# Kernel tuning notes

Measured on AMD Instinct MI355X. Metric: run time of the kernel, lower is better.

Reference implementation:

```python
import jax, jax.numpy as jnp
import numpy as np

B, T, HID = 2, 2048, 1024
H, DK, DV = 8, 128, 128      # num_heads, head_f_dim (key), head_i_dim (value)
LR = 128                     # gate low-rank dim
EPS = 1e-5


def setup_inputs() -> dict:
    key = jax.random.key(0)
    ks = jax.random.split(key, 8)
    def w(k, shape, fan_in):
        return jax.random.normal(k, shape, jnp.float32) / np.float32(np.sqrt(fan_in))
    return {
        "hidden_states": jax.random.normal(ks[0], (B, T, HID), jnp.float32),
        "Wq": w(ks[1], (HID, HID), HID),   # key_dim x hidden
        "Wk": w(ks[2], (HID, HID), HID),
        "Wv": w(ks[3], (HID, HID), HID),   # value_dim x hidden
        "Wg1": w(ks[4], (LR, HID), HID),   # low-rank gate down
        "Wg2": w(ks[5], (HID, LR), LR),    # low-rank gate up
        "g_norm_weight": jnp.ones((HID,), jnp.float32),
        "Wo": w(ks[6], (HID, HID), HID),
    }


def _lightnet_fwd(x, Wq, Wk, Wv, Wg1, Wg2, g_norm_weight, Wo):
    b, t, _ = x.shape
    q = jax.nn.silu(x @ Wq.T).reshape(b, t, H, DK)
    k = (x @ Wk.T).reshape(b, t, H, DK)
    v = (x @ Wv.T).reshape(b, t, H, DV)

    # LightNet gating: normalized keys via logcumsumexp over time
    z = jax.lax.cumlogsumexp(k, axis=1)                 # [b,t,h,dk]
    k = jnp.exp(k - z)                                  # exp-normalized keys
    g = jnp.concatenate([z[:, :1], z[:, :-1]], axis=1) - z  # <= 0; g[:,0]=0

    scale = DK ** -0.5

    # gated linear attention recurrence: S_t = exp(g_t) * S_{t-1} + k_t v_t^T
    def step(S, inp):
        qt, kt, vt, gt = inp                            # [b,h,dk],[b,h,dk],[b,h,dv],[b,h,dk]
        S = jnp.exp(gt)[..., None] * S + kt[..., None] * vt[..., None, :]
        o = jnp.einsum('bhk,bhkv->bhv', qt, S) * scale
        return S, o

    S0 = jnp.zeros((b, H, DK, DV), x.dtype)
    tfirst = lambda a: jnp.moveaxis(a, 1, 0)
    _, oT = jax.lax.scan(step, S0, (tfirst(q), tfirst(k), tfirst(v), tfirst(g)))
    o = jnp.moveaxis(oT, 0, 1).reshape(b, t, H * DV)    # [b,t,hidden]

    # RMSNorm(o) * swish(gate) then output projection
    gate = (x @ Wg1.T) @ Wg2.T
    o = o * jax.lax.rsqrt(jnp.mean(o * o, axis=-1, keepdims=True) + EPS) * g_norm_weight
    o = o * gate * jax.nn.sigmoid(gate)
    return o @ Wo.T


def reference(hidden_states, Wq, Wk, Wv, Wg1, Wg2, g_norm_weight, Wo):
    return _lightnet_fwd(hidden_states, Wq, Wk, Wv, Wg1, Wg2, g_norm_weight, Wo)
```

## Files before the change

### kernel.cpp

```cpp
#include <hip/hip_runtime.h>
#include <hip/hip_bf16.h>
#include <stdint.h>


typedef short short8 __attribute__((ext_vector_type(8)));
typedef float f32x4 __attribute__((ext_vector_type(4)));

#define T_SEQ 2048
#define HIDN  1024
#define SCALE 0.08838834764831845f
#define LDSP  136

__device__ __forceinline__ float blo(unsigned int u){
  union{unsigned int i; float f;} v; v.i = u << 16; return v.f;
}
__device__ __forceinline__ float bhi(unsigned int u){
  union{unsigned int i; float f;} v; v.i = u & 0xffff0000u; return v.f;
}
__device__ __forceinline__ float bu2f(unsigned short u){
  union{unsigned int i; float f;} v; v.i = ((unsigned int)u) << 16; return v.f;
}
__device__ __forceinline__ unsigned short f2bu(float f){
  union{float f; unsigned int i;} v; v.f = f;
  unsigned int x = v.i;
  x += 0x7fffu + ((x >> 16) & 1u);
  return (unsigned short)(x >> 16);
}
__device__ __forceinline__ void up8(const unsigned short* p, float* f){
  uint4 v = *(const uint4*)p;
  f[0]=blo(v.x); f[1]=bhi(v.x); f[2]=blo(v.y); f[3]=bhi(v.y);
  f[4]=blo(v.z); f[5]=bhi(v.z); f[6]=blo(v.w); f[7]=bhi(v.w);
}
__device__ __forceinline__ void async16(const void* g, void* l){
  __builtin_amdgcn_global_load_lds(
      (const __attribute__((address_space(1))) unsigned int*)g,
      (__attribute__((address_space(3))) unsigned int*)l, 16, 0, 0);
}

__global__ __launch_bounds__(256) void convert_all(
    const float* __restrict__ X,  const float* __restrict__ Wq,
    const float* __restrict__ Wk, const float* __restrict__ Wv,
    const float* __restrict__ Wg1,const float* __restrict__ Wg2,
    const float* __restrict__ gnw,const float* __restrict__ Wo,
    unsigned short* __restrict__ base)
{
  int q = blockIdx.x * 256 + threadIdx.x;
  const float* src; unsigned short* dst; int rel = q;
  if (rel < 1048576)            { src = X;   dst = base;            }
  else if ((rel -= 1048576) < 262144) { src = Wq;  dst = base + 4194304; }
  else if ((rel -=  262144) < 262144) { src = Wk;  dst = base + 5242880; }
  else if ((rel -=  262144) < 262144) { src = Wv;  dst = base + 6291456; }
  else if ((rel -=  262144) < 262144) { src = Wo;  dst = base + 7340032; }
  else if ((rel -=  262144) <  32768) { src = Wg1; dst = base + 8388608; }
  else if ((rel -=   32768) <  32768) { src = Wg2; dst = base + 8519680; }
  else   { rel -= 32768;                src = gnw; dst = base + 8650752; }
  float4 v = ((const float4*)src)[rel];
  ushort4 o; o.x=f2bu(v.x); o.y=f2bu(v.y); o.z=f2bu(v.z); o.w=f2bu(v.w);
  ((ushort4*)dst)[rel] = o;
}

__device__ __forceinline__ void gemm_core(
    const unsigned short* __restrict__ A, const unsigned short* __restrict__ B,
    int K, int row0, int col0,
    unsigned short* sA, unsigned short* sB, f32x4 acc[4][4], int tid)
{
  const int lane = tid & 63;
  const int wm = (tid >> 6) & 1, wn = tid >> 7;
  const int wb = tid & 192;
  for (int k0 = 0; k0 < K; k0 += 32){
    __syncthreads();
#pragma unroll
    for (int r = 0; r < 2; ++r){
      int idx  = r*256 + tid;
      int mrow = idx >> 2, kc = (idx & 3) * 8;
      async16(A + (size_t)(row0 + mrow)*K + k0 + kc, sA + (size_t)(r*256 + wb)*8);
      async16(B + (size_t)(col0 + mrow)*K + k0 + kc, sB + (size_t)(r*256 + wb)*8);
    }
    __syncthreads();
    short8 av[4], bv[4];
#pragma unroll
    for (int i=0;i<4;i++)
      av[i] = *(const short8*)(sA + (size_t)(wm*64 + i*16 + (lane&15))*32 + (lane>>4)*8);
#pragma unroll
    for (int j=0;j<4;j++)
      bv[j] = *(const short8*)(sB + (size_t)(wn*64 + j*16 + (lane&15))*32 + (lane>>4)*8);
#pragma unroll
    for (int i=0;i<4;i++)
#pragma unroll
      for (int j=0;j<4;j++)
        acc[i][j] = __builtin_amdgcn_mfma_f32_16x16x32_bf16(av[i], bv[j], acc[i][j], 0, 0, 0);
  }
}

__device__ __forceinline__ void epilogue_lds(
    f32x4 acc[4][4], int row0, int col0, int tid, int ldc, int act,
    unsigned short* __restrict__ Cb, unsigned short* sC)
{
  const int lane = tid & 63;
  const int wm = (tid >> 6) & 1, wn = tid >> 7;
#pragma unroll
  for (int p=0;p<4;p++){
    __syncthreads();
    if (wm == (p>>1)){
#pragma unroll
      for (int ii=0; ii<2; ii++){
        int i = (p&1)*2 + ii;
        int lr = i*16 + ((lane>>4)<<2) - (p&1)*32;
#pragma unroll
        for (int j=0;j<4;j++){
          int col = wn*64 + j*16 + (lane&15);
#pragma unroll
          for (int r=0;r<4;r++){
            float v = acc[i][j][r];
            if (act) v = v / (1.f + __expf(-v));
            sC[(lr+r)*128 + col] = f2bu(v);
          }
        }
      }
    }
    __syncthreads();
#pragma unroll
    for (int c = tid; c < 512; c += 256){
      int rr = c >> 4, off = (c & 15)*8;
      *(uint4*)&Cb[(size_t)(row0 + p*32 + rr)*ldc + col0 + off] =
          *(const uint4*)&sC[rr*128 + off];
    }
  }
}

__device__ __forceinline__ void epilogue_f32(
    f32x4 acc[4][4], int row0, int col0, int tid, int ldc,
    float* __restrict__ Cf)
{
  const int lane = tid & 63;
  const int wm = (tid >> 6) & 1, wn = tid >> 7;
#pragma unroll
  for (int i=0;i<4;i++){
    int rbase = row0 + wm*64 + i*16 + ((lane>>4)<<2);
#pragma unroll
    for (int j=0;j<4;j++){
      int col = col0 + wn*64 + j*16 + (lane&15);
#pragma unroll
      for (int r=0;r<4;r++)
        Cf[(size_t)(rbase + r)*ldc + col] = acc[i][j][r];
    }
  }
}

__global__ __launch_bounds__(256, 2) void proj_kernel(
    const unsigned short* __restrict__ X,
    const unsigned short* __restrict__ Wq, const unsigned short* __restrict__ Wk,
    const unsigned short* __restrict__ Wv, const unsigned short* __restrict__ Wg1,
    unsigned short* __restrict__ Qb, unsigned short* __restrict__ Kb,
    unsigned short* __restrict__ Vb, unsigned short* __restrict__ G1b)
{
  __shared__ unsigned short sA[128*32], sB[128*32];
  int tid = threadIdx.x;
  int which = blockIdx.y >> 3;
  const unsigned short* Bp = (which==0)?Wq:(which==1)?Wk:(which==2)?Wv:Wg1;
  int row0 = blockIdx.x * 128;
  int col0 = (which==3) ? 0 : (blockIdx.y & 7) * 128;
  f32x4 acc[4][4] = {};
  gemm_core(X, Bp, HIDN, row0, col0, sA, sB, acc, tid);
  if      (which==0) epilogue_lds(acc,row0,col0,tid,HIDN,1,Qb, sA);
  else if (which==1) epilogue_lds(acc,row0,col0,tid,HIDN,0,Kb, sA);
  else if (which==2) epilogue_lds(acc,row0,col0,tid,HIDN,0,Vb, sA);
  else               epilogue_lds(acc,row0,col0,tid,128 ,0,G1b,sA);
}

__global__ __launch_bounds__(256, 2) void gemm_bt(
    const unsigned short* __restrict__ A, const unsigned short* __restrict__ B,
    int K, int ldc, int act, float* __restrict__ Cf,
    unsigned short* __restrict__ Cb)
{
  __shared__ unsigned short sA[128*32], sB[128*32];
  int tid = threadIdx.x;
  int row0 = blockIdx.x * 128, col0 = blockIdx.y * 128;
  f32x4 acc[4][4] = {};
  gemm_core(A, B, K, row0, col0, sA, sB, acc, tid);
  if (Cb) epilogue_lds(acc, row0, col0, tid, ldc, act, Cb, sA);
  else    epilogue_f32(acc, row0, col0, tid, ldc, Cf);
}

__global__ __launch_bounds__(256) void attn_pass1(
    const unsigned short* __restrict__ Kb, const unsigned short* __restrict__ Vb,
    unsigned short* __restrict__ U, float* __restrict__ Esum)
{
  __shared__ unsigned short se[128*128];
  __shared__ unsigned short sv[128*128];
  int tid = threadIdx.x;
  int bh = blockIdx.x >> 4, ch = blockIdx.x & 15;
  int b = bh >> 3, h = bh & 7;
  size_t rowbase = (size_t)(b*T_SEQ + ch*128)*HIDN + h*128;

#pragma unroll
  for (int i=0;i<8;i++){
    int u = tid + i*256; int t = u >> 4, kc = (u & 15)*8;
    float kv[8]; up8(&Kb[rowbase + (size_t)t*HIDN + kc], kv);
    ushort4 a, c;
    a.x=f2bu(__expf(kv[0])); a.y=f2bu(__expf(kv[1]));
    a.z=f2bu(__expf(kv[2])); a.w=f2bu(__expf(kv[3]));
    c.x=f2bu(__expf(kv[4])); c.y=f2bu(__expf(kv[5]));
    c.z=f2bu(__expf(kv[6])); c.w=f2bu(__expf(kv[7]));
    *(ushort4*)&se[t*128 + kc    ] = a;
    *(ushort4*)&se[t*128 + kc + 4] = c;
  }
#pragma unroll
  for (int i=0;i<8;i++){
    int u = tid + i*256; int t = u >> 4, kc = (u & 15)*8;
    ((uint4*)sv)[u] = *(const uint4*)&Vb[rowbase + (size_t)t*HIDN + kc];
  }
  __syncthreads();

  if (tid < 128){
    float s = 0.f;
#pragma unroll 8
    for (int t=0;t<128;t++) s += bu2f(se[t*128 + tid]);
    Esum[(size_t)blockIdx.x*128 + tid] = s;
  }

  int kg = tid >> 4, vg = tid & 15;
  int k0 = kg*8, v0 = vg*8;
  float uacc[8][8] = {};
  for (int s=0;s<128;s++){
    float ev[8], vv[8];
    up8(&se[s*128 + k0], ev);
    up8(&sv[s*128 + v0], vv);
#pragma unroll
    for (int i=0;i<8;i++)
#pragma unroll
      for (int j=0;j<8;j++) uacc[i][j] += ev[i]*vv[j];
  }
  unsigned short* Ub = U + (size_t)blockIdx.x*16384;
#pragma unroll
  for (int j=0;j<8;j++){
    ushort4 w0, w1;
    w0.x=f2bu(uacc[0][j]); w0.y=f2bu(uacc[1][j]); w0.z=f2bu(uacc[2][j]); w0.w=f2bu(uacc[3][j]);
    w1.x=f2bu(uacc[4][j]); w1.y=f2bu(uacc[5][j]); w1.z=f2bu(uacc[6][j]); w1.w=f2bu(uacc[7][j]);
    *(ushort4*)&Ub[(v0+j)*128 + k0    ] = w0;
    *(ushort4*)&Ub[(v0+j)*128 + k0 + 4] = w1;
  }
}

__global__ __launch_bounds__(256) void attn_pass2(
    unsigned short* __restrict__ U, float* __restrict__ Esum)
{
  int bh = blockIdx.x >> 4, sl = blockIdx.x & 15;
  int p = sl*1024 + threadIdx.x*4;
  float r0=0.f, r1=0.f, r2=0.f, r3=0.f;
  for (int c=0;c<16;c++){
    ushort4* ptr = (ushort4*)&U[(size_t)(bh*16 + c)*16384 + p];
    ushort4 t = *ptr;
    ushort4 w;
    w.x=f2bu(r0); w.y=f2bu(r1); w.z=f2bu(r2); w.w=f2bu(r3);
    *ptr = w;
    r0 += bu2f(t.x); r1 += bu2f(t.y); r2 += bu2f(t.z); r3 += bu2f(t.w);
  }
  if (sl == 0 && threadIdx.x < 128){
    float r = 0.f;
    for (int c=0;c<16;c++){
      float* q = &Esum[(size_t)(bh*16 + c)*128 + threadIdx.x];
      float t = *q; *q = r; r += t;
    }
  }
}

__global__ __launch_bounds__(512, 2) void attn_pass3(
    const unsigned short* __restrict__ Kb, const unsigned short* __restrict__ Qb,
    const unsigned short* __restrict__ Vb, const unsigned short* __restrict__ U,
    const float* __restrict__ Esum, unsigned short* __restrict__ Oatt)
{
  __shared__ unsigned short smem[3*128*LDSP];
  __shared__ float seg_part[4*128];
  unsigned short* bufA = smem;
  unsigned short* bufB = smem + 128*LDSP;
  unsigned short* bufC = smem + 2*128*LDSP;

  int tid = threadIdx.x;
  const int lane = tid & 63, quad = lane >> 4;
  const int w = tid >> 6, wm = w & 3, wn = w >> 2;
  const int Rb = wm*32, Cb = wn*64;
  int bh = blockIdx.x >> 4, ch = blockIdx.x & 15;
  int b = bh >> 3, h = bh & 7;
  size_t rowbase = (size_t)(b*T_SEQ + ch*128)*HIDN + h*128;

#pragma unroll
  for (int i=0;i<4;i++){
    int u = tid + i*512; int t = u >> 4, kc = (u & 15)*8;
    *(uint4*)&bufA[t*LDSP + kc] = *(const uint4*)&Qb[rowbase + (size_t)t*HIDN + kc];
    float kv[8]; up8(&Kb[rowbase + (size_t)t*HIDN + kc], kv);
    ushort4 a, c;
    a.x=f2bu(__expf(kv[0])); a.y=f2bu(__expf(kv[1]));
    a.z=f2bu(__expf(kv[2])); a.w=f2bu(__expf(kv[3]));
    c.x=f2bu(__expf(kv[4])); c.y=f2bu(__expf(kv[5]));
    c.z=f2bu(__expf(kv[6])); c.w=f2bu(__expf(kv[7]));
    *(ushort4*)&bufB[t*LDSP + kc    ] = a;
    *(ushort4*)&bufB[t*LDSP + kc + 4] = c;
    *(uint4*)&bufC[t*LDSP + kc] =
        *(const uint4*)&U[(size_t)blockIdx.x*16384 + (size_t)t*128 + kc];
  }
  __syncthreads();

  {
    int col = tid & 127, seg = tid >> 7;
    float psum = 0.f;
    for (int s = seg*32; s < seg*32+32; ++s) psum += bu2f(bufB[s*LDSP + col]);
    seg_part[seg*128 + col] = psum;
    __syncthreads();
    float run = Esum[(size_t)blockIdx.x*128 + col];
    for (int ss=0; ss<4; ++ss) if (ss < seg) run += seg_part[ss*128 + col];
    for (int s = seg*32; s < seg*32+32; ++s){
      run += bu2f(bufB[s*LDSP + col]);
      float q = bu2f(bufA[s*LDSP + col]);
      bufA[s*LDSP + col] = f2bu(q * SCALE * __builtin_amdgcn_rcpf(run));
    }
  }
  __syncthreads();

  f32x4 accO[2][4] = {}, accP[2][4] = {};
  short8 av[2], bv[4];
#pragma unroll
  for (int k0=0; k0<128; k0+=32){
#pragma unroll
    for (int i=0;i<2;i++)
      av[i] = *(const short8*)(bufA + (Rb + i*16 + (lane&15))*LDSP + k0 + quad*8);
#pragma unroll
    for (int j=0;j<4;j++)
      bv[j] = *(const short8*)(bufC + (Cb + j*16 + (lane&15))*LDSP + k0 + quad*8);
#pragma unroll
    for (int i=0;i<2;i++)
#pragma unroll
      for (int j=0;j<4;j++)
        accO[i][j] = __builtin_amdgcn_mfma_f32_16x16x32_bf16(av[i], bv[j], accO[i][j], 0,0,0);
#pragma unroll
    for (int j=0;j<4;j++)
      bv[j] = *(const short8*)(bufB + (Cb + j*16 + (lane&15))*LDSP + k0 + quad*8);
#pragma unroll
    for (int i=0;i<2;i++)
#pragma unroll
      for (int j=0;j<4;j++)
        accP[i][j] = __builtin_amdgcn_mfma_f32_16x16x32_bf16(av[i], bv[j], accP[i][j], 0,0,0);
  }
  __syncthreads();

#pragma unroll
  for (int i=0;i<2;i++){
#pragma unroll
    for (int j=0;j<4;j++){
      int s = Cb + j*16 + (lane&15);
#pragma unroll
      for (int r=0;r<4;r++){
        int t = Rb + i*16 + quad*4 + r;
        bufA[t*LDSP + s] = f2bu(s <= t ? accP[i][j][r] : 0.f);
      }
    }
  }
#pragma unroll
  for (int i=0;i<4;i++){
    int u = tid + i*512; int t = u >> 4, kc = (u & 15)*8;
    unsigned short tmp[8];
    *(uint4*)tmp = *(const uint4*)&Vb[rowbase + (size_t)t*HIDN + kc];
#pragma unroll
    for (int j=0;j<8;j++) bufB[(kc+j)*LDSP + t] = tmp[j];
  }
  __syncthreads();

#pragma unroll
  for (int k0=0; k0<128; k0+=32){
#pragma unroll
    for (int i=0;i<2;i++)
      av[i] = *(const short8*)(bufA + (Rb + i*16 + (lane&15))*LDSP + k0 + quad*8);
#pragma unroll
    for (int j=0;j<4;j++)
      bv[j] = *(const short8*)(bufB + (Cb + j*16 + (lane&15))*LDSP + k0 + quad*8);
#pragma unroll
    for (int i=0;i<2;i++)
#pragma unroll
      for (int j=0;j<4;j++)
        accO[i][j] = __builtin_amdgcn_mfma_f32_16x16x32_bf16(av[i], bv[j], accO[i][j], 0,0,0);
  }
  __syncthreads();

#pragma unroll
  for (int i=0;i<2;i++){
#pragma unroll
    for (int j=0;j<4;j++){
      int v = Cb + j*16 + (lane&15);
#pragma unroll
      for (int r=0;r<4;r++){
        int t = Rb + i*16 + quad*4 + r;
        bufC[t*LDSP + v] = f2bu(accO[i][j][r]);
      }
    }
  }
  __syncthreads();
#pragma unroll
  for (int i=0;i<4;i++){
    int u = tid + i*512; int t = u >> 4, kc = (u & 15)*8;
    *(uint4*)&Oatt[rowbase + (size_t)t*HIDN + kc] = *(const uint4*)&bufC[t*LDSP + kc];
  }
}

__global__ __launch_bounds__(256) void norm_gate(
    const unsigned short* __restrict__ Oatt, const unsigned short* __restrict__ Gt,
    const unsigned short* __restrict__ gnw, unsigned short* __restrict__ Onorm)
{
  int row = blockIdx.x, tid = threadIdx.x;
  ushort4 o4 = *(const ushort4*)&Oatt[(size_t)row*HIDN + tid*4];
  float ox = bu2f(o4.x), oy = bu2f(o4.y), oz = bu2f(o4.z), ow = bu2f(o4.w);
  float ss = ox*ox + oy*oy + oz*oz + ow*ow;
#pragma unroll
  for (int off=32; off>0; off>>=1) ss += __shfl_down(ss, off, 64);
  __shared__ float red[4];
  if ((tid & 63) == 0) red[tid>>6] = ss;
  __syncthreads();
  float rstd = rsqrtf((red[0]+red[1]+red[2]+red[3]) * (1.f/1024.f) + 1e-5f);
  ushort4 g4 = *(const ushort4*)&Gt[(size_t)row*HIDN + tid*4];
  ushort4 w4 = *(const ushort4*)&gnw[tid*4];
  ushort4 r4;
  r4.x = f2bu(ox * rstd * bu2f(w4.x) * bu2f(g4.x));
  r4.y = f2bu(oy * rstd * bu2f(w4.y) * bu2f(g4.y));
  r4.z = f2bu(oz * rstd * bu2f(w4.z) * bu2f(g4.z));
  r4.w = f2bu(ow * rstd * bu2f(w4.w) * bu2f(g4.w));
  *(ushort4*)&Onorm[(size_t)row*HIDN + tid*4] = r4;
}

extern "C" void kernel_launch(void* const* d_in, const int* in_sizes, int n_in,
                              void* d_out, int out_size, void* d_ws, size_t ws_size,
                              hipStream_t stream) {
  unsigned short* wsS = (unsigned short*)d_ws;

  unsigned short* Xc   = wsS;
  unsigned short* Wqc  = wsS + 4194304;
  unsigned short* Wkc  = wsS + 5242880;
  unsigned short* Wvc  = wsS + 6291456;
  unsigned short* Woc  = wsS + 7340032;
  unsigned short* Wg1c = wsS + 8388608;
  unsigned short* Wg2c = wsS + 8519680;
  unsigned short* gnwc = wsS + 8650752;
  unsigned short* Qb   = wsS + 8651776;
  unsigned short* Kb   = wsS + 12846080;
  unsigned short* Vb   = wsS + 17040384;
  unsigned short* G1b  = wsS + 21234688;
  unsigned short* Gt   = wsS + 21758976;
  unsigned short* Ub   = wsS + 25953280;
  unsigned short* Oattb= wsS + 30147584;
  float*          Esum = (float*)(wsS + 34341888);
  unsigned short* Onorm = Qb;

  convert_all<<<8449, 256, 0, stream>>>(
      (const float*)d_in[0], (const float*)d_in[1], (const float*)d_in[2],
      (const float*)d_in[3], (const float*)d_in[4], (const float*)d_in[5],
      (const float*)d_in[6], (const float*)d_in[7], wsS);

  proj_kernel<<<dim3(32,25), 256, 0, stream>>>(Xc, Wqc, Wkc, Wvc, Wg1c, Qb, Kb, Vb, G1b);
  gemm_bt   <<<dim3(32,8),  256, 0, stream>>>(G1b, Wg2c, 128, HIDN, 1, nullptr, Gt);
  attn_pass1<<<256, 256, 0, stream>>>(Kb, Vb, Ub, Esum);
  attn_pass2<<<256, 256, 0, stream>>>(Ub, Esum);
  attn_pass3<<<256, 512, 0, stream>>>(Kb, Qb, Vb, Ub, Esum, Oattb);
  norm_gate <<<4096, 256, 0, stream>>>(Oattb, Gt, gnwc, Onorm);
  gemm_bt   <<<dim3(32,8),  256, 0, stream>>>(Onorm, Woc, HIDN, HIDN, 0,
                                              (float*)d_out, nullptr);
}
```

Baseline: 223.5 us.

## Fuse RMSNorm-gate into output GEMM, MFMA-ize chunk state pass, widen GEMM K-tile

The output GEMM now applies the RMSNorm, gnorm weight and gate while staging its A operand. The per-row sum of squares is accumulated with atomics in attn_pass3, and convert_all zeroes the buffer first, so the separate norm_gate kernel and its round trip through global memory go away. attn_pass1's chunk outer product is rewritten from scalar FMA loops over LDS into MFMA on transposed tiles with 512 threads. The shared GEMM core loads a 64-wide K tile per barrier pair instead of 32, halving the number of syncs. Costs: the A tile in out_gemm is loaded synchronously with elementwise math, LDS per block doubles in the GEMMs, and atomic accumulation makes the sum-of-squares order non-deterministic.

Result: no change. 223.6 us (+0.1%).

```diff
diff --git a/kernel.cpp b/kernel.cpp
--- a/kernel.cpp
+++ b/kernel.cpp
@@ -42,7 +42,7 @@
     const float* __restrict__ Wk, const float* __restrict__ Wv,
     const float* __restrict__ Wg1,const float* __restrict__ Wg2,
     const float* __restrict__ gnw,const float* __restrict__ Wo,
-    unsigned short* __restrict__ base)
+    unsigned short* __restrict__ base, float* __restrict__ SumSq)
 {
   int q = blockIdx.x * 256 + threadIdx.x;
   const float* src; unsigned short* dst; int rel = q;
@@ -53,7 +53,9 @@
   else if ((rel -=  262144) < 262144) { src = Wo;  dst = base + 7340032; }
   else if ((rel -=  262144) <  32768) { src = Wg1; dst = base + 8388608; }
   else if ((rel -=   32768) <  32768) { src = Wg2; dst = base + 8519680; }
-  else   { rel -= 32768;                src = gnw; dst = base + 8650752; }
+  else if ((rel -=   32768) <    256) { src = gnw; dst = base + 8650752; }
+  else { rel -= 256;
+    ((float4*)SumSq)[rel] = make_float4(0.f,0.f,0.f,0.f); return; }
   float4 v = ((const float4*)src)[rel];
   ushort4 o; o.x=f2bu(v.x); o.y=f2bu(v.y); o.z=f2bu(v.z); o.w=f2bu(v.w);
   ((ushort4*)dst)[rel] = o;
@@ -67,28 +69,36 @@
   const int lane = tid & 63;
   const int wm = (tid >> 6) & 1, wn = tid >> 7;
   const int wb = tid & 192;
-  for (int k0 = 0; k0 < K; k0 += 32){
-    __syncthreads();
-#pragma unroll
-    for (int r = 0; r < 2; ++r){
-      int idx  = r*256 + tid;
-      int mrow = idx >> 2, kc = (idx & 3) * 8;
-      async16(A + (size_t)(row0 + mrow)*K + k0 + kc, sA + (size_t)(r*256 + wb)*8);
-      async16(B + (size_t)(col0 + mrow)*K + k0 + kc, sB + (size_t)(r*256 + wb)*8);
-    }
-    __syncthreads();
-    short8 av[4], bv[4];
-#pragma unroll
-    for (int i=0;i<4;i++)
-      av[i] = *(const short8*)(sA + (size_t)(wm*64 + i*16 + (lane&15))*32 + (lane>>4)*8);
-#pragma unroll
-    for (int j=0;j<4;j++)
-      bv[j] = *(const short8*)(sB + (size_t)(wn*64 + j*16 + (lane&15))*32 + (lane>>4)*8);
-#pragma unroll
-    for (int i=0;i<4;i++)
+  for (int k0 = 0; k0 < K; k0 += 64){
+    __syncthreads();
+#pragma unroll
+    for (int h = 0; h < 2; ++h){
+#pragma unroll
+      for (int r = 0; r < 2; ++r){
+        int idx  = r*256 + tid;
+        int mrow = idx >> 2, kc = (idx & 3) * 8;
+        async16(A + (size_t)(row0 + mrow)*K + k0 + h*32 + kc,
+                sA + (size_t)(h*512 + r*256 + wb)*8);
+        async16(B + (size_t)(col0 + mrow)*K + k0 + h*32 + kc,
+                sB + (size_t)(h*512 + r*256 + wb)*8);
+      }
+    }
+    __syncthreads();
+#pragma unroll
+    for (int h = 0; h < 2; ++h){
+      short8 av[4], bv[4];
+#pragma unroll
+      for (int i=0;i<4;i++)
+        av[i] = *(const short8*)(sA + h*4096 + (size_t)(wm*64 + i*16 + (lane&15))*32 + (lane>>4)*8);
 #pragma unroll
       for (int j=0;j<4;j++)
-        acc[i][j] = __builtin_amdgcn_mfma_f32_16x16x32_bf16(av[i], bv[j], acc[i][j], 0, 0, 0);
+        bv[j] = *(const short8*)(sB + h*4096 + (size_t)(wn*64 + j*16 + (lane&15))*32 + (lane>>4)*8);
+#pragma unroll
+      for (int i=0;i<4;i++)
+#pragma unroll
+        for (int j=0;j<4;j++)
+          acc[i][j] = __builtin_amdgcn_mfma_f32_16x16x32_bf16(av[i], bv[j], acc[i][j], 0, 0, 0);
+    }
   }
 }
 
@@ -154,7 +164,7 @@
     unsigned short* __restrict__ Qb, unsigned short* __restrict__ Kb,
     unsigned short* __restrict__ Vb, unsigned short* __restrict__ G1b)
 {
-  __shared__ unsigned short sA[128*32], sB[128*32];
+  __shared__ unsigned short sA[128*64], sB[128*64];
   int tid = threadIdx.x;
   int which = blockIdx.y >> 3;
   const unsigned short* Bp = (which==0)?Wq:(which==1)?Wk:(which==2)?Wv:Wg1;
@@ -170,75 +180,143 @@
 
 __global__ __launch_bounds__(256, 2) void gemm_bt(
     const unsigned short* __restrict__ A, const unsigned short* __restrict__ B,
-    int K, int ldc, int act, float* __restrict__ Cf,
-    unsigned short* __restrict__ Cb)
-{
-  __shared__ unsigned short sA[128*32], sB[128*32];
+    int K, int ldc, int act, unsigned short* __restrict__ Cb)
+{
+  __shared__ unsigned short sA[128*64], sB[128*64];
   int tid = threadIdx.x;
   int row0 = blockIdx.x * 128, col0 = blockIdx.y * 128;
   f32x4 acc[4][4] = {};
   gemm_core(A, B, K, row0, col0, sA, sB, acc, tid);
-  if (Cb) epilogue_lds(acc, row0, col0, tid, ldc, act, Cb, sA);
-  else    epilogue_f32(acc, row0, col0, tid, ldc, Cf);
-}
-
-__global__ __launch_bounds__(256) void attn_pass1(
+  epilogue_lds(acc, row0, col0, tid, ldc, act, Cb, sA);
+}
+
+__global__ __launch_bounds__(256, 2) void out_gemm(
+    const unsigned short* __restrict__ Oatt, const unsigned short* __restrict__ Gt,
+    const unsigned short* __restrict__ gnw,  const float* __restrict__ SumSq,
+    const unsigned short* __restrict__ Wo,   float* __restrict__ Out)
+{
+  __shared__ unsigned short sA[128*64], sB[128*64];
+  int tid = threadIdx.x;
+  int row0 = blockIdx.x * 128, col0 = blockIdx.y * 128;
+  const int wb = tid & 192;
+  f32x4 acc[4][4] = {};
+  const int lane = tid & 63;
+  const int wm = (tid >> 6) & 1, wn = tid >> 7;
+  for (int k0 = 0; k0 < HIDN; k0 += 64){
+    __syncthreads();
+#pragma unroll
+    for (int h = 0; h < 2; ++h){
+#pragma unroll
+      for (int r = 0; r < 2; ++r){
+        int idx  = r*256 + tid;
+        int mrow = idx >> 2, kc = (idx & 3) * 8;
+        async16(Wo + (size_t)(col0 + mrow)*HIDN + k0 + h*32 + kc,
+                sB + (size_t)(h*512 + r*256 + wb)*8);
+        int grow = row0 + mrow, gcol = k0 + h*32 + kc;
+        float o[8], g[8], w[8];
+        up8(&Oatt[(size_t)grow*HIDN + gcol], o);
+        up8(&Gt  [(size_t)grow*HIDN + gcol], g);
+        up8(&gnw[gcol], w);
+        float rstd = rsqrtf(SumSq[grow]*(1.f/1024.f) + 1e-5f);
+        unsigned short a8[8];
+#pragma unroll
+        for (int j=0;j<8;j++) a8[j] = f2bu(o[j]*rstd*w[j]*g[j]);
+        *(uint4*)(sA + (size_t)(h*4096 + mrow*32 + kc)) = *(const uint4*)a8;
+      }
+    }
+    __syncthreads();
+#pragma unroll
+    for (int h = 0; h < 2; ++h){
+      short8 av[4], bv[4];
+#pragma unroll
+      for (int i=0;i<4;i++)
+        av[i] = *(const short8*)(sA + h*4096 + (size_t)(wm*64 + i*16 + (lane&15))*32 + (lane>>4)*8);
+#pragma unroll
+      for (int j=0;j<4;j++)
+        bv[j] = *(const short8*)(sB + h*4096 + (size_t)(wn*64 + j*16 + (lane&15))*32 + (lane>>4)*8);
+#pragma unroll
+      for (int i=0;i<4;i++)
+#pragma unroll
+        for (int j=0;j<4;j++)
+          acc[i][j] = __builtin_amdgcn_mfma_f32_16x16x32_bf16(av[i], bv[j], acc[i][j], 0, 0, 0);
+    }
+  }
+  epilogue_f32(acc, row0, col0, tid, HIDN, Out);
+}
+
+__global__ __launch_bounds__(512, 2) void attn_pass1(
     const unsigned short* __restrict__ Kb, const unsigned short* __restrict__ Vb,
     unsigned short* __restrict__ U, float* __restrict__ Esum)
 {
-  __shared__ unsigned short se[128*128];
-  __shared__ unsigned short sv[128*128];
+  __shared__ unsigned short Vt[128*LDSP], Et[128*LDSP];
+  __shared__ float seg_part[4*128];
   int tid = threadIdx.x;
+  const int lane = tid & 63, quad = lane >> 4;
+  const int w = tid >> 6, wm = w & 3, wn = w >> 2;
+  const int Rb = wm*32, Cb = wn*64;
   int bh = blockIdx.x >> 4, ch = blockIdx.x & 15;
   int b = bh >> 3, h = bh & 7;
   size_t rowbase = (size_t)(b*T_SEQ + ch*128)*HIDN + h*128;
 
 #pragma unroll
-  for (int i=0;i<8;i++){
-    int u = tid + i*256; int t = u >> 4, kc = (u & 15)*8;
+  for (int i=0;i<4;i++){
+    int u = tid + i*512; int t = u >> 4, kc = (u & 15)*8;
+    unsigned short tmp[8];
+    *(uint4*)tmp = *(const uint4*)&Vb[rowbase + (size_t)t*HIDN + kc];
+#pragma unroll
+    for (int j=0;j<8;j++) Vt[(kc+j)*LDSP + t] = tmp[j];
     float kv[8]; up8(&Kb[rowbase + (size_t)t*HIDN + kc], kv);
-    ushort4 a, c;
-    a.x=f2bu(__expf(kv[0])); a.y=f2bu(__expf(kv[1]));
-    a.z=f2bu(__expf(kv[2])); a.w=f2bu(__expf(kv[3]));
-    c.x=f2bu(__expf(kv[4])); c.y=f2bu(__expf(kv[5]));
-    c.z=f2bu(__expf(kv[6])); c.w=f2bu(__expf(kv[7]));
-    *(ushort4*)&se[t*128 + kc    ] = a;
-    *(ushort4*)&se[t*128 + kc + 4] = c;
-  }
-#pragma unroll
-  for (int i=0;i<8;i++){
-    int u = tid + i*256; int t = u >> 4, kc = (u & 15)*8;
-    ((uint4*)sv)[u] = *(const uint4*)&Vb[rowbase + (size_t)t*HIDN + kc];
-  }
-  __syncthreads();
-
-  if (tid < 128){
+#pragma unroll
+    for (int j=0;j<8;j++) Et[(kc+j)*LDSP + t] = f2bu(__expf(kv[j]));
+  }
+  __syncthreads();
+
+  {
+    int seg = tid >> 7, k = tid & 127;
     float s = 0.f;
-#pragma unroll 8
-    for (int t=0;t<128;t++) s += bu2f(se[t*128 + tid]);
-    Esum[(size_t)blockIdx.x*128 + tid] = s;
-  }
-
-  int kg = tid >> 4, vg = tid & 15;
-  int k0 = kg*8, v0 = vg*8;
-  float uacc[8][8] = {};
-  for (int s=0;s<128;s++){
-    float ev[8], vv[8];
-    up8(&se[s*128 + k0], ev);
-    up8(&sv[s*128 + v0], vv);
-#pragma unroll
-    for (int i=0;i<8;i++)
-#pragma unroll
-      for (int j=0;j<8;j++) uacc[i][j] += ev[i]*vv[j];
-  }
+    for (int c = seg*32; c < seg*32+32; ++c) s += bu2f(Et[k*LDSP + c]);
+    seg_part[seg*128 + k] = s;
+  }
+  __syncthreads();
+  if (tid < 128)
+    Esum[(size_t)blockIdx.x*128 + tid] =
+        seg_part[tid] + seg_part[128+tid] + seg_part[256+tid] + seg_part[384+tid];
+
+  f32x4 acc[2][4] = {};
+  short8 av[2], bv[4];
+#pragma unroll
+  for (int s0=0; s0<128; s0+=32){
+#pragma unroll
+    for (int i=0;i<2;i++)
+      av[i] = *(const short8*)(Vt + (Rb + i*16 + (lane&15))*LDSP + s0 + quad*8);
+#pragma unroll
+    for (int j=0;j<4;j++)
+      bv[j] = *(const short8*)(Et + (Cb + j*16 + (lane&15))*LDSP + s0 + quad*8);
+#pragma unroll
+    for (int i=0;i<2;i++)
+#pragma unroll
+      for (int j=0;j<4;j++)
+        acc[i][j] = __builtin_amdgcn_mfma_f32_16x16x32_bf16(av[i], bv[j], acc[i][j], 0,0,0);
+  }
+  __syncthreads();
+
+#pragma unroll
+  for (int i=0;i<2;i++)
+#pragma unroll
+    for (int j=0;j<4;j++){
+      int k = Cb + j*16 + (lane&15);
+#pragma unroll
+      for (int r=0;r<4;r++){
+        int v = Rb + i*16 + quad*4 + r;
+        Et[v*LDSP + k] = f2bu(acc[i][j][r]);
+      }
+    }
+  __syncthreads();
   unsigned short* Ub = U + (size_t)blockIdx.x*16384;
 #pragma unroll
-  for (int j=0;j<8;j++){
-    ushort4 w0, w1;
-    w0.x=f2bu(uacc[0][j]); w0.y=f2bu(uacc[1][j]); w0.z=f2bu(uacc[2][j]); w0.w=f2bu(uacc[3][j]);
-    w1.x=f2bu(uacc[4][j]); w1.y=f2bu(uacc[5][j]); w1.z=f2bu(uacc[6][j]); w1.w=f2bu(uacc[7][j]);
-    *(ushort4*)&Ub[(v0+j)*128 + k0    ] = w0;
-    *(ushort4*)&Ub[(v0+j)*128 + k0 + 4] = w1;
+  for (int i=0;i<4;i++){
+    int u = tid + i*512; int v = u >> 4, kc = (u & 15)*8;
+    *(uint4*)&Ub[v*128 + kc] = *(const uint4*)&Et[v*LDSP + kc];
   }
 }
 
@@ -268,7 +346,8 @@
 __global__ __launch_bounds__(512, 2) void attn_pass3(
     const unsigned short* __restrict__ Kb, const unsigned short* __restrict__ Qb,
     const unsigned short* __restrict__ Vb, const unsigned short* __restrict__ U,
-    const float* __restrict__ Esum, unsigned short* __restrict__ Oatt)
+    const float* __restrict__ Esum, unsigned short* __restrict__ Oatt,
+    float* __restrict__ SumSq)
 {
   __shared__ unsigned short smem[3*128*LDSP];
   __shared__ float seg_part[4*128];
@@ -394,35 +473,25 @@
     }
   }
   __syncthreads();
+
+  {
+    int seg = tid >> 7, row = tid & 127;
+    float s = 0.f;
+    for (int c = seg*32; c < seg*32+32; ++c){
+      float x = bu2f(bufC[row*LDSP + c]); s += x*x;
+    }
+    seg_part[seg*128 + row] = s;
+  }
 #pragma unroll
   for (int i=0;i<4;i++){
     int u = tid + i*512; int t = u >> 4, kc = (u & 15)*8;
     *(uint4*)&Oatt[rowbase + (size_t)t*HIDN + kc] = *(const uint4*)&bufC[t*LDSP + kc];
   }
-}
-
-__global__ __launch_bounds__(256) void norm_gate(
-    const unsigned short* __restrict__ Oatt, const unsigned short* __restrict__ Gt,
-    const unsigned short* __restrict__ gnw, unsigned short* __restrict__ Onorm)
-{
-  int row = blockIdx.x, tid = threadIdx.x;
-  ushort4 o4 = *(const ushort4*)&Oatt[(size_t)row*HIDN + tid*4];
-  float ox = bu2f(o4.x), oy = bu2f(o4.y), oz = bu2f(o4.z), ow = bu2f(o4.w);
-  float ss = ox*ox + oy*oy + oz*oz + ow*ow;
-#pragma unroll
-  for (int off=32; off>0; off>>=1) ss += __shfl_down(ss, off, 64);
-  __shared__ float red[4];
-  if ((tid & 63) == 0) red[tid>>6] = ss;
-  __syncthreads();
-  float rstd = rsqrtf((red[0]+red[1]+red[2]+red[3]) * (1.f/1024.f) + 1e-5f);
-  ushort4 g4 = *(const ushort4*)&Gt[(size_t)row*HIDN + tid*4];
-  ushort4 w4 = *(const ushort4*)&gnw[tid*4];
-  ushort4 r4;
-  r4.x = f2bu(ox * rstd * bu2f(w4.x) * bu2f(g4.x));
-  r4.y = f2bu(oy * rstd * bu2f(w4.y) * bu2f(g4.y));
-  r4.z = f2bu(oz * rstd * bu2f(w4.z) * bu2f(g4.z));
-  r4.w = f2bu(ow * rstd * bu2f(w4.w) * bu2f(g4.w));
-  *(ushort4*)&Onorm[(size_t)row*HIDN + tid*4] = r4;
+  __syncthreads();
+  if (tid < 128){
+    float s = seg_part[tid] + seg_part[128+tid] + seg_part[256+tid] + seg_part[384+tid];
+    atomicAdd(&SumSq[(size_t)b*T_SEQ + ch*128 + tid], s);
+  }
 }
 
 extern "C" void kernel_launch(void* const* d_in, const int* in_sizes, int n_in,
@@ -446,19 +515,18 @@
   unsigned short* Ub   = wsS + 25953280;
   unsigned short* Oattb= wsS + 30147584;
   float*          Esum = (float*)(wsS + 34341888);
-  unsigned short* Onorm = Qb;
-
-  convert_all<<<8449, 256, 0, stream>>>(
+  float*          SumSq= (float*)(wsS + 34407424);
+
+  convert_all<<<8453, 256, 0, stream>>>(
       (const float*)d_in[0], (const float*)d_in[1], (const float*)d_in[2],
       (const float*)d_in[3], (const float*)d_in[4], (const float*)d_in[5],
-      (const float*)d_in[6], (const float*)d_in[7], wsS);
+      (const float*)d_in[6], (const float*)d_in[7], wsS, SumSq);
 
   proj_kernel<<<dim3(32,25), 256, 0, stream>>>(Xc, Wqc, Wkc, Wvc, Wg1c, Qb, Kb, Vb, G1b);
-  gemm_bt   <<<dim3(32,8),  256, 0, stream>>>(G1b, Wg2c, 128, HIDN, 1, nullptr, Gt);
-  attn_pass1<<<256, 256, 0, stream>>>(Kb, Vb, Ub, Esum);
+  gemm_bt   <<<dim3(32,8),  256, 0, stream>>>(G1b, Wg2c, 128, HIDN, 1, Gt);
+  attn_pass1<<<256, 512, 0, stream>>>(Kb, Vb, Ub, Esum);
   attn_pass2<<<256, 256, 0, stream>>>(Ub, Esum);
-  attn_pass3<<<256, 512, 0, stream>>>(Kb, Qb, Vb, Ub, Esum, Oattb);
-  norm_gate <<<4096, 256, 0, stream>>>(Oattb, Gt, gnwc, Onorm);
-  gemm_bt   <<<dim3(32,8),  256, 0, stream>>>(Onorm, Woc, HIDN, HIDN, 0,
-                                              (float*)d_out, nullptr);
-}
+  attn_pass3<<<256, 512, 0, stream>>>(Kb, Qb, Vb, Ub, Esum, Oattb, SumSq);
+  out_gemm  <<<dim3(32,8),  256, 0, stream>>>(Oattb, Gt, gnwc, SumSq, Woc,
+                                              (float*)d_out);
+}
```
